# Kernel tuning notes

Measured on AMD Instinct MI355X. Metric: run time of the kernel, lower is better.

Reference implementation:

```python
import jax, jax.numpy as jnp
import numpy as np

NEG_SLOPE = 0.01  # torch F.leaky_relu default


def _leaky_relu(v):
    return jnp.where(v >= 0, v, NEG_SLOPE * v)


def _att_layer(t, w1, w2):
    # t: [b, c, n] ; SE-style channel attention with scalar gate
    y = t.mean(axis=-1)                                   # [b, c] (AdaptiveAvgPool1d(1))
    y = jax.nn.sigmoid(jax.nn.relu(y @ w1.T) @ w2.T)       # [b, 1]
    return t * y[:, :, None]


def _avwgcn(x, node_emb, supports, cheb, wpool, bpool, iw, ib, gw, gb,
            a1w1, a1w2, a2w1, a2w2):
    # x: [b, n, c_in]; supports/cheb: [k, n, n]
    b, n, _ = x.shape
    weights = jnp.einsum('nd,dkio->nkio', node_emb, wpool)   # per-node dyn weights
    bias = node_emb @ bpool                                  # [n, o]
    x_g = jnp.einsum('knm,bmc->bnkc', supports, x)           # [b, n, k, c_in]
    x_gconv0 = jnp.einsum('bnki,nkio->bno', x_g, weights) + bias
    x0 = x @ iw.T + ib                                       # init_gconv: [b, n, o]
    x_g1 = jnp.einsum('knm,bmc->bnkc', cheb, x0).reshape(b, n, -1)
    x_gconv1 = x_g1 @ gw.T + gb                              # [b, n, o]
    out = (_att_layer(_leaky_relu(x_gconv0).transpose(0, 2, 1), a1w1, a1w2)
           + _att_layer(_leaky_relu(x_gconv1).transpose(0, 2, 1), a2w1, a2w2))
    return out.transpose(0, 2, 1)                            # [b, n, o]


def _cheb_supports(L, k):
    n = L.shape[0]
    s = [jnp.eye(n, dtype=L.dtype), L]
    for _ in range(2, k):
        s.append(2.0 * L @ s[-1] - s[-2])
    return jnp.stack(s, axis=0)  # [k, n, n]


B, N, DIN, DOUT, K, ED = 64, 1024, 32, 64, 3, 16
CIN = DIN + DOUT  # 96 (gate/update input = cat(x, state))


def setup_inputs() -> dict:
    key = jax.random.key(0)
    ks = jax.random.split(key, 32)
    g = lambda i, shape, s=0.1: jax.random.normal(ks[i], shape, dtype=jnp.float32) * s
    inp = {
        'x': jax.random.normal(ks[0], (B, N, DIN), dtype=jnp.float32),
        'state': jax.random.normal(ks[1], (B, N, DOUT), dtype=jnp.float32),
        'node_embeddings': jax.random.normal(ks[2], (N, ED), dtype=jnp.float32),
        'learned_tilde': jax.random.normal(ks[3], (N, N), dtype=jnp.float32) / np.sqrt(N),
        'cheb_polynomials': jax.random.normal(ks[4], (K, N, N), dtype=jnp.float32) / np.sqrt(N),
        # gate AVWGCN: dim_in=96, dim_out=2*DOUT=128
        'gate_wpool': g(5, (ED, K, CIN, 2 * DOUT)),
        'gate_bpool': g(6, (ED, 2 * DOUT)),
        'gate_iw': g(7, (2 * DOUT, CIN)), 'gate_ib': g(8, (2 * DOUT,)),
        'gate_gw': g(9, (2 * DOUT, 2 * DOUT * K)), 'gate_gb': g(10, (2 * DOUT,)),
        'gate_a1w1': g(11, (2 * DOUT // 16, 2 * DOUT)), 'gate_a1w2': g(12, (1, 2 * DOUT // 16)),
        'gate_a2w1': g(13, (2 * DOUT // 16, 2 * DOUT)), 'gate_a2w2': g(14, (1, 2 * DOUT // 16)),
        # update AVWGCN: dim_in=96, dim_out=DOUT=64
        'upd_wpool': g(15, (ED, K, CIN, DOUT)),
        'upd_bpool': g(16, (ED, DOUT)),
        'upd_iw': g(17, (DOUT, CIN)), 'upd_ib': g(18, (DOUT,)),
        'upd_gw': g(19, (DOUT, DOUT * K)), 'upd_gb': g(20, (DOUT,)),
        'upd_a1w1': g(21, (DOUT // 16, DOUT)), 'upd_a1w2': g(22, (1, DOUT // 16)),
        'upd_a2w1': g(23, (DOUT // 16, DOUT)), 'upd_a2w2': g(24, (1, DOUT // 16)),
    }
    return inp


def reference(x, state, node_embeddings, learned_tilde, cheb_polynomials,
              gate_wpool, gate_bpool, gate_iw, gate_ib, gate_gw, gate_gb,
              gate_a1w1, gate_a1w2, gate_a2w1, gate_a2w2,
              upd_wpool, upd_bpool, upd_iw, upd_ib, upd_gw, upd_gb,
              upd_a1w1, upd_a1w2, upd_a2w1, upd_a2w2):
    supports = _cheb_supports(learned_tilde, K)  # [k, n, n]
    inp_state = jnp.concatenate([x, state], axis=-1)  # [b, n, din+dout]
    z_r = jax.nn.sigmoid(_avwgcn(inp_state, node_embeddings, supports, cheb_polynomials,
                                 gate_wpool, gate_bpool, gate_iw, gate_ib, gate_gw, gate_gb,
                                 gate_a1w1, gate_a1w2, gate_a2w1, gate_a2w2))
    z, r = jnp.split(z_r, 2, axis=-1)
    candidate = jnp.concatenate([x, z * state], axis=-1)
    hc = jnp.tanh(_avwgcn(candidate, node_embeddings, supports, cheb_polynomials,
                          upd_wpool, upd_bpool, upd_iw, upd_ib, upd_gw, upd_gb,
                          upd_a1w1, upd_a1w2, upd_a2w1, upd_a2w2))
    h = r * state + (1.0 - r) * hc
    return h
```

## Files before the change

kernel.cpp:

```cpp
#include <hip/hip_runtime.h>
#include <hip/hip_bf16.h>
#include <math.h>


#define B_  64
#define N_  1024
#define CIN_ 96
#define R_  288

typedef __attribute__((ext_vector_type(8))) short bf16x8;
typedef __attribute__((ext_vector_type(4))) float f32x4;
typedef unsigned short u16;
typedef unsigned int u32;

__device__ __forceinline__ float lrelu(float v) { return v >= 0.f ? v : 0.01f * v; }
__device__ __forceinline__ float sigmoidf_(float u) { return 1.f / (1.f + expf(-u)); }
__device__ __forceinline__ u16 f2b(float f) {
  union { float f; u32 u; } c; c.f = f;
  u32 u = c.u;
  return (u16)((u + 0x7FFFu + ((u >> 16) & 1u)) >> 16);
}
__device__ __forceinline__ float b2f(u16 u) {
  union { u32 x; float f; } c; c.x = ((u32)u) << 16; return c.f;
}
__device__ __forceinline__ void gload_lds16(const u16* gp, u16* lp) {
  __builtin_amdgcn_global_load_lds((const __attribute__((address_space(1))) u32*)gp,
                                   (__attribute__((address_space(3))) u32*)lp, 16, 0, 0);
}

__global__ __launch_bounds__(256) void concat_bf2(const float* __restrict__ x,
                                                  const float* __restrict__ st,
                                                  float* __restrict__ inp,
                                                  u16* __restrict__ inpb) {
  size_t t = (size_t)blockIdx.x * 256 + threadIdx.x;
  if (t >= (size_t)B_ * N_ * CIN_) return;
  int i = (int)(t % CIN_);
  size_t v = t / CIN_;
  size_t b = v & 63, n = v >> 6;
  float f = (i < 32) ? x[(b * N_ + n) * 32 + i] : st[(b * N_ + n) * 64 + (i - 32)];
  inp[t] = f;
  inpb[t] = f2b(f);
}

__global__ __launch_bounds__(256) void conv_f2b(const float* __restrict__ in,
                                                u16* __restrict__ out, int n4) {
  int t = blockIdx.x * 256 + threadIdx.x;
  if (t >= n4) return;
  float4 v = ((const float4*)in)[t];
  ushort4 o;
  o.x = f2b(v.x); o.y = f2b(v.y); o.z = f2b(v.z); o.w = f2b(v.w);
  ((ushort4*)out)[t] = o;
}

__global__ __launch_bounds__(256) void split_hilo(const float* __restrict__ in,
                                                  u16* __restrict__ hi,
                                                  u16* __restrict__ lo, int n4) {
  int t = blockIdx.x * 256 + threadIdx.x;
  if (t >= n4) return;
  float4 v = ((const float4*)in)[t];
  ushort4 h, l;
  h.x = f2b(v.x); l.x = f2b(v.x - b2f(h.x));
  h.y = f2b(v.y); l.y = f2b(v.y - b2f(h.y));
  h.z = f2b(v.z); l.z = f2b(v.z - b2f(h.z));
  h.w = f2b(v.w); l.w = f2b(v.w - b2f(h.w));
  ((ushort4*)hi)[t] = h;
  ((ushort4*)lo)[t] = l;
}

__global__ __launch_bounds__(256) void transpose_split(const float* __restrict__ in,
                                                       u16* __restrict__ hiT,
                                                       u16* __restrict__ loT) {
  __shared__ float t[32][33];
  const int tid = threadIdx.x;
  const int j0 = blockIdx.x * 32, r0 = blockIdx.y * 32;
  const int tc = tid & 31, tr = tid >> 5;
#pragma unroll
  for (int q = 0; q < 4; ++q)
    t[tr + q * 8][tc] = in[(size_t)(r0 + tr + q * 8) * 1024 + j0 + tc];
  __syncthreads();
  const int jj = tid >> 3, rq = (tid & 7) * 4;
  ushort4 h, l;
#pragma unroll
  for (int q = 0; q < 4; ++q) {
    float v = t[rq + q][jj];
    u16 hh = f2b(v);
    ((u16*)&h)[q] = hh;
    ((u16*)&l)[q] = f2b(v - b2f(hh));
  }
  *(ushort4*)(hiT + (size_t)(j0 + jj) * N_ + r0 + rq) = h;
  *(ushort4*)(loT + (size_t)(j0 + jj) * N_ + r0 + rq) = l;
}

__global__ __launch_bounds__(256) void transpose_b2b(const u16* __restrict__ Z, int Zs,
                                                     int Ctot, u16* __restrict__ Zt) {
  __shared__ u16 t[32][36];
  const int tid = threadIdx.x;
  const int c0 = blockIdx.x * 32, n0 = blockIdx.y * 32, b = blockIdx.z;
  {
    const int i = tid >> 3, c4 = (tid & 7) * 4;
    ushort4 v = *(const ushort4*)(Z + ((size_t)(n0 + i) * 64 + b) * Zs + c0 + c4);
    t[i][c4] = v.x; t[i][c4 + 1] = v.y; t[i][c4 + 2] = v.z; t[i][c4 + 3] = v.w;
  }
  __syncthreads();
  {
    const int c = tid >> 3, n4 = (tid & 7) * 4;
    ushort4 o;
    o.x = t[n4][c]; o.y = t[n4 + 1][c]; o.z = t[n4 + 2][c]; o.w = t[n4 + 3][c];
    *(ushort4*)(Zt + (size_t)(b * Ctot + c0 + c) * 1024 + n0 + n4) = o;
  }
}

__global__ __launch_bounds__(256) void mfma_l2p(const u16* __restrict__ Lhi,
                                                const u16* __restrict__ Llo,
                                                const u16* __restrict__ LhiT,
                                                const u16* __restrict__ LloT,
                                                float* __restrict__ P) {
  __shared__ u16 Asl[64 * 64];
  __shared__ u16 Bsl[64 * 64];
  const int tid = threadIdx.x;
  const int w = tid >> 6, lane = tid & 63;
  const int m0 = blockIdx.y * 64, n0 = blockIdx.x * 64;
  const int ph = blockIdx.z;
  const int wr = w >> 1, wc = w & 1;
  const int sr = lane >> 3, so = lane & 7;
  const int cl = lane & 15, q4 = lane >> 4;
  f32x4 acc[2][2] = {};

  const u16* A = (ph == 1) ? Llo : Lhi;
  const u16* B = (ph == 2) ? LloT : LhiT;
  for (int k0 = 0; k0 < 1024; k0 += 64) {
    __syncthreads();
#pragma unroll
    for (int i = 0; i < 2; ++i) {
      const int r = i * 32 + w * 8 + sr;
      const int o = so ^ (r & 7);
      gload_lds16(A + (size_t)(m0 + r) * 1024 + k0 + o * 8, Asl + (i * 32 + w * 8) * 64);
      gload_lds16(B + (size_t)(n0 + r) * 1024 + k0 + o * 8, Bsl + (i * 32 + w * 8) * 64);
    }
    __syncthreads();
#pragma unroll
    for (int kk = 0; kk < 2; ++kk) {
      bf16x8 af[2], bfr[2];
#pragma unroll
      for (int mi = 0; mi < 2; ++mi) {
        const int ra = wr * 32 + mi * 16 + cl;
        af[mi] = *(const bf16x8*)(Asl + ra * 64 + ((kk * 4 + q4) ^ (ra & 7)) * 8);
      }
#pragma unroll
      for (int ni = 0; ni < 2; ++ni) {
        const int rb = wc * 32 + ni * 16 + cl;
        bfr[ni] = *(const bf16x8*)(Bsl + rb * 64 + ((kk * 4 + q4) ^ (rb & 7)) * 8);
      }
#pragma unroll
      for (int mi = 0; mi < 2; ++mi)
#pragma unroll
        for (int ni = 0; ni < 2; ++ni)
          acc[mi][ni] = __builtin_amdgcn_mfma_f32_16x16x32_bf16(af[mi], bfr[ni], acc[mi][ni], 0, 0, 0);
    }
  }
  float* Pz = P + ((size_t)ph << 20);
#pragma unroll
  for (int mi = 0; mi < 2; ++mi)
#pragma unroll
    for (int ni = 0; ni < 2; ++ni) {
      const int j = n0 + wc * 32 + ni * 16 + cl;
#pragma unroll
      for (int r = 0; r < 4; ++r) {
        const int m = m0 + wr * 32 + mi * 16 + q4 * 4 + r;
        Pz[(size_t)m * 1024 + j] = acc[mi][ni][r];
      }
    }
}

__global__ __launch_bounds__(256) void l2_finish(const float* __restrict__ P,
                                                 u16* __restrict__ Y) {
  int t = blockIdx.x * 256 + threadIdx.x;
  float4 a = ((const float4*)P)[t];
  float4 b = ((const float4*)(P + 1048576))[t];
  float4 c = ((const float4*)(P + 2097152))[t];
  int e = t << 2;
  int m = e >> 10, j = e & 1023;
  ushort4 o;
  o.x = f2b(2.f * (a.x + b.x + c.x) - (m == j     ? 1.f : 0.f));
  o.y = f2b(2.f * (a.y + b.y + c.y) - (m == j + 1 ? 1.f : 0.f));
  o.z = f2b(2.f * (a.z + b.z + c.z) - (m == j + 2 ? 1.f : 0.f));
  o.w = f2b(2.f * (a.w + b.w + c.w) - (m == j + 3 ? 1.f : 0.f));
  ((ushort4*)Y)[t] = o;
}

__global__ __launch_bounds__(256) void mfma_stack_f32(const u16* __restrict__ A,
                                                      const u16* __restrict__ Bt,
                                                      float* __restrict__ Y, int J) {
  __shared__ u16 Asl[2][128 * 32];
  __shared__ u16 Bsl[2][128 * 32];
  const int tid = threadIdx.x;
  const int w = tid >> 6, lane = tid & 63;
  const int m0 = blockIdx.y * 128, n0 = blockIdx.x * 128;
  const int wr = w >> 1, wc = w & 1;
  const int sr = lane >> 2, so = lane & 3;
  const int cl = lane & 15, q4 = lane >> 4;
  f32x4 acc[4][4] = {};

  auto STAGE = [&](u16* Ad, u16* Bd, int k0) {
#pragma unroll
    for (int i = 0; i < 2; ++i) {
      const int r = i * 64 + w * 16 + sr;
      const int o = so ^ ((r >> 1) & 3);
      gload_lds16(A + (size_t)(m0 + r) * 1024 + k0 + o * 8, Ad + (i * 64 + w * 16) * 32);
      gload_lds16(Bt + (size_t)(n0 + r) * 1024 + k0 + o * 8, Bd + (i * 64 + w * 16) * 32);
    }
  };
  auto COMPUTE = [&](const u16* As, const u16* Bs) {
    bf16x8 af[4], bfr[4];
#pragma unroll
    for (int mi = 0; mi < 4; ++mi) {
      const int ra = wr * 64 + mi * 16 + cl;
      af[mi] = *(const bf16x8*)(As + ra * 32 + (q4 ^ ((ra >> 1) & 3)) * 8);
    }
#pragma unroll
    for (int ni = 0; ni < 4; ++ni) {
      const int rb = wc * 64 + ni * 16 + cl;
      bfr[ni] = *(const bf16x8*)(Bs + rb * 32 + (q4 ^ ((rb >> 1) & 3)) * 8);
    }
#pragma unroll
    for (int mi = 0; mi < 4; ++mi)
#pragma unroll
      for (int ni = 0; ni < 4; ++ni)
        acc[mi][ni] = __builtin_amdgcn_mfma_f32_16x16x32_bf16(af[mi], bfr[ni], acc[mi][ni], 0, 0, 0);
  };

  STAGE(Asl[0], Bsl[0], 0);
  for (int k0 = 0; k0 < 1024; k0 += 64) {
    STAGE(Asl[1], Bsl[1], k0 + 32);
    asm volatile("s_waitcnt vmcnt(4)" ::: "memory");
    __builtin_amdgcn_s_barrier();
    __builtin_amdgcn_sched_barrier(0);
    COMPUTE(Asl[0], Bsl[0]);
    asm volatile("s_waitcnt lgkmcnt(0)" ::: "memory");
    __builtin_amdgcn_s_barrier();
    __builtin_amdgcn_sched_barrier(0);
    if (k0 + 64 < 1024) {
      STAGE(Asl[0], Bsl[0], k0 + 64);
      asm volatile("s_waitcnt vmcnt(4)" ::: "memory");
    } else {
      asm volatile("s_waitcnt vmcnt(0)" ::: "memory");
    }
    __builtin_amdgcn_s_barrier();
    __builtin_amdgcn_sched_barrier(0);
    COMPUTE(Asl[1], Bsl[1]);
    asm volatile("s_waitcnt lgkmcnt(0)" ::: "memory");
    __builtin_amdgcn_s_barrier();
    __builtin_amdgcn_sched_barrier(0);
  }
#pragma unroll
  for (int mi = 0; mi < 4; ++mi)
#pragma unroll
    for (int ni = 0; ni < 4; ++ni) {
      const int j = n0 + wc * 64 + ni * 16 + cl;
#pragma unroll
      for (int r = 0; r < 4; ++r) {
        const int m = m0 + wr * 64 + mi * 16 + q4 * 4 + r;
        Y[(size_t)m * J + j] = acc[mi][ni][r];
      }
    }
}

template <int O, int OSH>
__global__ __launch_bounds__(128) void vgen2(const float* __restrict__ gw,
                                             const float* __restrict__ iw,
                                             const float* __restrict__ ib,
                                             int Ctot,
                                             u16* __restrict__ Vb,
                                             float* __restrict__ ball) {
  const int c = blockIdx.x;
  const int col = threadIdx.x;
  if (c >= Ctot) {
    if (col < 96) Vb[(size_t)c * 96 + col] = 0;
    else if (col == 96) ball[c] = 0.f;
    return;
  }
  __shared__ float sg[O];
  const int o = c & (O - 1), k = c >> OSH;
  const float* g = gw + (size_t)o * (3 * O) + (size_t)k * O;
  for (int e = col; e < O; e += 128) sg[e] = g[e];
  __syncthreads();
  if (col < 96) {
    float s = 0.f;
#pragma unroll
    for (int j = 0; j < O; ++j) s += sg[j] * iw[j * 96 + col];
    Vb[(size_t)c * 96 + col] = f2b(s);
  } else if (col == 96) {
    float s = 0.f;
#pragma unroll
    for (int j = 0; j < O; ++j) s += sg[j] * ib[j];
    ball[c] = s;
  }
}

__global__ __launch_bounds__(256) void zgemm(const u16* __restrict__ A,
                                             const u16* __restrict__ Bt,
                                             const float* __restrict__ ball,
                                             u16* __restrict__ Z, int Zs) {
  __shared__ u16 Asl[128 * 32];
  __shared__ u16 Bsl[128 * 32];
  const int tid = threadIdx.x;
  const int w = tid >> 6, lane = tid & 63;
  const int m0 = blockIdx.y * 128, n0 = blockIdx.x * 128;
  const int wr = w >> 1, wc = w & 1;
  const int sr = lane >> 2, so = lane & 3;
  const int cl = lane & 15, q4 = lane >> 4;
  f32x4 acc[4][4] = {};
  for (int k0 = 0; k0 < 96; k0 += 32) {
    __syncthreads();
#pragma unroll
    for (int i = 0; i < 2; ++i) {
      const int r = i * 64 + w * 16 + sr;
      const int o = so ^ (r & 3);
      gload_lds16(A + (size_t)(m0 + r) * 96 + k0 + o * 8, Asl + (i * 64 + w * 16) * 32);
      gload_lds16(Bt + (size_t)(n0 + r) * 96 + k0 + o * 8, Bsl + (i * 64 + w * 16) * 32);
    }
    __syncthreads();
    bf16x8 af[4], bfr[4];
#pragma unroll
    for (int mi = 0; mi < 4; ++mi) {
      const int ra = wr * 64 + mi * 16 + cl;
      af[mi] = *(const bf16x8*)(Asl + ra * 32 + (q4 ^ (ra & 3)) * 8);
    }
#pragma unroll
    for (int ni = 0; ni < 4; ++ni) {
      const int rb = wc * 64 + ni * 16 + cl;
      bfr[ni] = *(const bf16x8*)(Bsl + rb * 32 + (q4 ^ (rb & 3)) * 8);
    }
#pragma unroll
    for (int mi = 0; mi < 4; ++mi)
#pragma unroll
      for (int ni = 0; ni < 4; ++ni)
        acc[mi][ni] = __builtin_amdgcn_mfma_f32_16x16x32_bf16(af[mi], bfr[ni], acc[mi][ni], 0, 0, 0);
  }
#pragma unroll
  for (int mi = 0; mi < 4; ++mi)
#pragma unroll
    for (int ni = 0; ni < 4; ++ni) {
      const int c = n0 + wc * 64 + ni * 16 + cl;
      const float bb = ball[c];
#pragma unroll
      for (int r = 0; r < 4; ++r) {
        const int m = m0 + wr * 64 + mi * 16 + q4 * 4 + r;
        Z[(size_t)m * Zs + c] = f2b(acc[mi][ni][r] + bb);
      }
    }
}

__global__ __launch_bounds__(512) void mfma_k3(const u16* __restrict__ A3,
                                               const u16* __restrict__ Zt,
                                               const float* __restrict__ gb,
                                               float* __restrict__ Y,
                                               int J, int obits) {
  __shared__ u16 Asl[2][128 * 64];
  __shared__ u16 Bsl[2][128 * 64];
  const int tid = threadIdx.x;
  const int w = tid >> 6, lane = tid & 63;
  const int m0 = blockIdx.y * 128, n0 = blockIdx.x * 128;
  const int wr = w >> 2, wc = w & 3;
  const int sr = lane >> 3, so = lane & 7;
  const int cl = lane & 15, q4 = lane >> 4;
  const int omask = (1 << obits) - 1;
  f32x4 acc[4][2] = {};

  auto STAGE = [&](u16* Ad, u16* Bd, int k0) {
    const int kb = k0 >> 10, ko = k0 & 1023;
#pragma unroll
    for (int i = 0; i < 2; ++i) {
      const int r = i * 64 + w * 8 + sr;
      const int o = so ^ (r & 7);
      gload_lds16(A3 + (size_t)kb * 1048576 + (size_t)(m0 + r) * 1024 + ko + o * 8,
                  Ad + (i * 64 + w * 8) * 64);
      const int jp = n0 + r;
      const int brow = (((jp >> obits) * 3 + kb) << obits) | (jp & omask);
      gload_lds16(Zt + (size_t)brow * 1024 + ko + o * 8, Bd + (i * 64 + w * 8) * 64);
    }
  };
  auto COMPUTE = [&](const u16* As, const u16* Bs) {
#pragma unroll
    for (int kk = 0; kk < 2; ++kk) {
      bf16x8 af[4], bfr[2];
#pragma unroll
      for (int mi = 0; mi < 4; ++mi) {
        const int ra = wr * 64 + mi * 16 + cl;
        af[mi] = *(const bf16x8*)(As + ra * 64 + ((kk * 4 + q4) ^ (ra & 7)) * 8);
      }
#pragma unroll
      for (int ni = 0; ni < 2; ++ni) {
        const int rb = wc * 32 + ni * 16 + cl;
        bfr[ni] = *(const bf16x8*)(Bs + rb * 64 + ((kk * 4 + q4) ^ (rb & 7)) * 8);
      }
#pragma unroll
      for (int mi = 0; mi < 4; ++mi)
#pragma unroll
        for (int ni = 0; ni < 2; ++ni)
          acc[mi][ni] = __builtin_amdgcn_mfma_f32_16x16x32_bf16(af[mi], bfr[ni], acc[mi][ni], 0, 0, 0);
    }
  };

  STAGE(Asl[0], Bsl[0], 0);
  for (int k0 = 0; k0 < 3072; k0 += 128) {
    STAGE(Asl[1], Bsl[1], k0 + 64);
    asm volatile("s_waitcnt vmcnt(4)" ::: "memory");
    __builtin_amdgcn_s_barrier();
    __builtin_amdgcn_sched_barrier(0);
    COMPUTE(Asl[0], Bsl[0]);
    asm volatile("s_waitcnt lgkmcnt(0)" ::: "memory");
    __builtin_amdgcn_s_barrier();
    __builtin_amdgcn_sched_barrier(0);
    if (k0 + 128 < 3072) {
      STAGE(Asl[0], Bsl[0], k0 + 128);
      asm volatile("s_waitcnt vmcnt(4)" ::: "memory");
    } else {
      asm volatile("s_waitcnt vmcnt(0)" ::: "memory");
    }
    __builtin_amdgcn_s_barrier();
    __builtin_amdgcn_sched_barrier(0);
    COMPUTE(Asl[1], Bsl[1]);
    asm volatile("s_waitcnt lgkmcnt(0)" ::: "memory");
    __builtin_amdgcn_s_barrier();
    __builtin_amdgcn_sched_barrier(0);
  }
#pragma unroll
  for (int mi = 0; mi < 4; ++mi)
#pragma unroll
    for (int ni = 0; ni < 2; ++ni) {
      const int j = n0 + wc * 32 + ni * 16 + cl;
      const float bb = gb[j & omask];
#pragma unroll
      for (int r = 0; r < 4; ++r) {
        const int m = m0 + wr * 64 + mi * 16 + q4 * 4 + r;
        Y[(size_t)m * J + j] = acc[mi][ni][r] + bb;
      }
    }
}

__global__ __launch_bounds__(512) void mfma_k3w(const u16* __restrict__ A3,
                                                const u16* __restrict__ Zt,
                                                const float* __restrict__ gb,
                                                float* __restrict__ Y,
                                                int J, int obits) {
  __shared__ u16 Asl[2][128 * 64];
  __shared__ u16 Bsl[2][256 * 64];
  const int tid = threadIdx.x;
  const int w = tid >> 6, lane = tid & 63;
  const int m0 = blockIdx.y * 128, n0 = blockIdx.x * 256;
  const int wr = w >> 2, wc = w & 3;
  const int sr = lane >> 3, so = lane & 7;
  const int cl = lane & 15, q4 = lane >> 4;
  const int omask = (1 << obits) - 1;
  f32x4 acc[4][4] = {};

  auto STAGE = [&](u16* Ad, u16* Bd, int k0) {
    const int kb = k0 >> 10, ko = k0 & 1023;
#pragma unroll
    for (int i = 0; i < 2; ++i) {
      const int r = i * 64 + w * 8 + sr;
      const int o = so ^ (r & 7);
      gload_lds16(A3 + (size_t)kb * 1048576 + (size_t)(m0 + r) * 1024 + ko + o * 8,
                  Ad + (i * 64 + w * 8) * 64);
    }
#pragma unroll
    for (int i = 0; i < 4; ++i) {
      const int r = i * 64 + w * 8 + sr;
      const int o = so ^ (r & 7);
      const int jp = n0 + r;
      const int brow = (((jp >> obits) * 3 + kb) << obits) | (jp & omask);
      gload_lds16(Zt + (size_t)brow * 1024 + ko + o * 8, Bd + (i * 64 + w * 8) * 64);
    }
  };
  auto COMPUTE = [&](const u16* As, const u16* Bs) {
#pragma unroll
    for (int kk = 0; kk < 2; ++kk) {
      bf16x8 af[4], bfr[4];
#pragma unroll
      for (int mi = 0; mi < 4; ++mi) {
        const int ra = wr * 64 + mi * 16 + cl;
        af[mi] = *(const bf16x8*)(As + ra * 64 + ((kk * 4 + q4) ^ (ra & 7)) * 8);
      }
#pragma unroll
      for (int ni = 0; ni < 4; ++ni) {
        const int rb = wc * 64 + ni * 16 + cl;
        bfr[ni] = *(const bf16x8*)(Bs + rb * 64 + ((kk * 4 + q4) ^ (rb & 7)) * 8);
      }
#pragma unroll
      for (int mi = 0; mi < 4; ++mi)
#pragma unroll
        for (int ni = 0; ni < 4; ++ni)
          acc[mi][ni] = __builtin_amdgcn_mfma_f32_16x16x32_bf16(af[mi], bfr[ni], acc[mi][ni], 0, 0, 0);
    }
  };

  STAGE(Asl[0], Bsl[0], 0);
  for (int k0 = 0; k0 < 3072; k0 += 128) {
    STAGE(Asl[1], Bsl[1], k0 + 64);
    asm volatile("s_waitcnt vmcnt(6)" ::: "memory");
    __builtin_amdgcn_s_barrier();
    __builtin_amdgcn_sched_barrier(0);
    COMPUTE(Asl[0], Bsl[0]);
    asm volatile("s_waitcnt lgkmcnt(0)" ::: "memory");
    __builtin_amdgcn_s_barrier();
    __builtin_amdgcn_sched_barrier(0);
    if (k0 + 128 < 3072) {
      STAGE(Asl[0], Bsl[0], k0 + 128);
      asm volatile("s_waitcnt vmcnt(6)" ::: "memory");
    } else {
      asm volatile("s_waitcnt vmcnt(0)" ::: "memory");
    }
    __builtin_amdgcn_s_barrier();
    __builtin_amdgcn_sched_barrier(0);
    COMPUTE(Asl[1], Bsl[1]);
    asm volatile("s_waitcnt lgkmcnt(0)" ::: "memory");
    __builtin_amdgcn_s_barrier();
    __builtin_amdgcn_sched_barrier(0);
  }
#pragma unroll
  for (int mi = 0; mi < 4; ++mi)
#pragma unroll
    for (int ni = 0; ni < 4; ++ni) {
      const int j = n0 + wc * 64 + ni * 16 + cl;
      const float bb = gb[j & omask];
#pragma unroll
      for (int r = 0; r < 4; ++r) {
        const int m = m0 + wr * 64 + mi * 16 + q4 * 4 + r;
        Y[(size_t)m * J + j] = acc[mi][ni][r] + bb;
      }
    }
}

template <int OW>
__global__ __launch_bounds__(256) void weightgen3w(const float* __restrict__ emb,
                                                   const float* __restrict__ wpool,
                                                   u16* __restrict__ W) {
  const int tid = threadIdx.x;
  const int ro = blockIdx.x * 256 + tid;
  const int r = ro / OW, o = ro % OW;
  const int n0 = blockIdx.y * 64;
  __shared__ float semb[64][17];
  for (int e = tid; e < 1024; e += 256) semb[e >> 4][e & 15] = emb[(n0 + (e >> 4)) * 16 + (e & 15)];
  __syncthreads();
  float wv[16];
#pragma unroll
  for (int d = 0; d < 16; ++d) wv[d] = wpool[((size_t)d * R_ + r) * OW + o];
#pragma unroll 4
  for (int n = 0; n < 64; ++n) {
    float s = 0.f;
#pragma unroll
    for (int d = 0; d < 16; ++d) s += semb[n][d] * wv[d];
    W[(size_t)(n0 + n) * (R_ * OW) + ro] = f2b(s);
  }
}

template <int OW>
__global__ __launch_bounds__(256) void pernode9(const float* __restrict__ xa,
                                                const float* __restrict__ xbc,
                                                const u16* __restrict__ W,
                                                const float* __restrict__ emb,
                                                const float* __restrict__ bpool,
                                                float* __restrict__ outp) {
  constexpr int QO = OW / 32;
  const int n = blockIdx.x;
  const int tid = threadIdx.x;
  __shared__ __align__(16) float sW[32][OW + 4];
  __shared__ __align__(16) float sX[32][68];
  __shared__ float semb[16];
  if (tid < 16) semb[tid] = emb[n * 16 + tid];
  const int tx = tid & 31, tb = tid >> 5;
  const int lb = tid >> 2, li = (tid & 3) * 8;
  float acc[8][QO] = {};
  const u16* Wn = W + (size_t)n * (R_ * OW);

  for (int c = 0; c < 9; ++c) {
    const int k = c / 3, i0 = (c % 3) * 32;
    const float* xk = (k == 0) ? (xa + (size_t)n * 6144)
                               : (xbc + ((size_t)(k - 1) * 1024 + n) * 6144);
    __syncthreads();
    {
#pragma unroll
      for (int it = 0; it < OW / 64; ++it) {
        const int slot = it * 256 + tid;
        const int row = slot / (OW / 8), o8 = (slot % (OW / 8)) * 8;
        uint4 v = *(const uint4*)(Wn + (size_t)(c * 32 + row) * OW + o8);
        sW[row][o8 + 0] = b2f((u16)(v.x & 0xFFFF)); sW[row][o8 + 1] = b2f((u16)(v.x >> 16));
        sW[row][o8 + 2] = b2f((u16)(v.y & 0xFFFF)); sW[row][o8 + 3] = b2f((u16)(v.y >> 16));
        sW[row][o8 + 4] = b2f((u16)(v.z & 0xFFFF)); sW[row][o8 + 5] = b2f((u16)(v.z >> 16));
        sW[row][o8 + 6] = b2f((u16)(v.w & 0xFFFF)); sW[row][o8 + 7] = b2f((u16)(v.w >> 16));
      }
    }
    {
      const float* p = xk + (size_t)lb * 96 + i0 + li;
      float4 v0 = *(const float4*)p;
      float4 v1 = *(const float4*)(p + 4);
      sX[li + 0][lb] = v0.x; sX[li + 1][lb] = v0.y;
      sX[li + 2][lb] = v0.z; sX[li + 3][lb] = v0.w;
      sX[li + 4][lb] = v1.x; sX[li + 5][lb] = v1.y;
      sX[li + 6][lb] = v1.z; sX[li + 7][lb] = v1.w;
    }
    __syncthreads();
#pragma unroll
    for (int il = 0; il < 32; ++il) {
      float4 xv0 = *(const float4*)&sX[il][tb * 8];
      float4 xv1 = *(const float4*)&sX[il][tb * 8 + 4];
      float xv[8] = {xv0.x, xv0.y, xv0.z, xv0.w, xv1.x, xv1.y, xv1.z, xv1.w};
      float wv[QO];
      if constexpr (QO == 4) {
        float4 w4 = *(const float4*)&sW[il][tx * 4];
        wv[0] = w4.x; wv[1] = w4.y; wv[2] = w4.z; wv[3] = w4.w;
      } else {
        float2 w2 = *(const float2*)&sW[il][tx * 2];
        wv[0] = w2.x; wv[1] = w2.y;
      }
#pragma unroll
      for (int j = 0; j < 8; ++j)
#pragma unroll
        for (int q = 0; q < QO; ++q) acc[j][q] += xv[j] * wv[q];
    }
  }
  float bias[QO];
#pragma unroll
  for (int q = 0; q < QO; ++q) {
    int o = tx * QO + q;
    float s = 0.f;
#pragma unroll
    for (int d = 0; d < 16; ++d) s += semb[d] * bpool[d * OW + o];
    bias[q] = s;
  }
#pragma unroll
  for (int j = 0; j < 8; ++j) {
    size_t base = ((size_t)n * B_ + tb * 8 + j) * OW + tx * QO;
#pragma unroll
    for (int q = 0; q < QO; ++q) outp[base + q] = acc[j][q] + bias[q];
  }
}

template <int C>
__global__ __launch_bounds__(256) void att_reduce(const float* __restrict__ A0,
                                                  const float* __restrict__ A1,
                                                  float* __restrict__ part0,
                                                  float* __restrict__ part1) {
  constexpr int C4 = C / 4;
  constexpr int H = 256 / C4;
  const int chunk = blockIdx.x;
  const int b = blockIdx.y;
  const int tid = threadIdx.x;
  const int c4 = tid % C4, h = tid / C4;
  __shared__ float4 r0[256], r1[256];
  float4 s0 = {0.f, 0.f, 0.f, 0.f}, s1 = {0.f, 0.f, 0.f, 0.f};
  const float4* p0 = (const float4*)(A0 + (size_t)b * C) + c4;
  const float4* p1 = (const float4*)(A1 + (size_t)b * C) + c4;
  const size_t stride = (size_t)B_ * C4;
  for (int n = chunk * 64 + h; n < chunk * 64 + 64; n += H) {
    float4 v0 = p0[(size_t)n * stride];
    float4 v1 = p1[(size_t)n * stride];
    s0.x += lrelu(v0.x); s0.y += lrelu(v0.y); s0.z += lrelu(v0.z); s0.w += lrelu(v0.w);
    s1.x += lrelu(v1.x); s1.y += lrelu(v1.y); s1.z += lrelu(v1.z); s1.w += lrelu(v1.w);
  }
  r0[tid] = s0; r1[tid] = s1;
  __syncthreads();
  if (h == 0) {
    for (int hh = 1; hh < H; ++hh) {
      float4 a = r0[c4 + hh * C4], bb = r1[c4 + hh * C4];
      s0.x += a.x; s0.y += a.y; s0.z += a.z; s0.w += a.w;
      s1.x += bb.x; s1.y += bb.y; s1.z += bb.z; s1.w += bb.w;
    }
    ((float4*)(part0 + ((size_t)b * 16 + chunk) * C))[c4] = s0;
    ((float4*)(part1 + ((size_t)b * 16 + chunk) * C))[c4] = s1;
  }
}

template <int C, int HID>
__global__ __launch_bounds__(256) void att_finish(const float* __restrict__ part0,
                                                  const float* __restrict__ part1,
                                                  const float* __restrict__ w11,
                                                  const float* __restrict__ w12,
                                                  const float* __restrict__ w21,
                                                  const float* __restrict__ w22,
                                                  float* __restrict__ sout) {
  const int b = blockIdx.x;
  const int tid = threadIdx.x;
  __shared__ float sm0[C], sm1[C];
  __shared__ float h0[HID], h1[HID];
  if (tid < C) {
    float s0 = 0.f, s1 = 0.f;
    for (int ch = 0; ch < 16; ++ch) {
      s0 += part0[((size_t)b * 16 + ch) * C + tid];
      s1 += part1[((size_t)b * 16 + ch) * C + tid];
    }
    sm0[tid] = s0 * (1.f / N_); sm1[tid] = s1 * (1.f / N_);
  }
  __syncthreads();
  if (tid < HID) {
    float a = 0.f;
    for (int cc = 0; cc < C; ++cc) a += sm0[cc] * w11[tid * C + cc];
    h0[tid] = fmaxf(a, 0.f);
  } else if (tid >= 32 && tid < 32 + HID) {
    int j = tid - 32;
    float a = 0.f;
    for (int cc = 0; cc < C; ++cc) a += sm1[cc] * w21[j * C + cc];
    h1[j] = fmaxf(a, 0.f);
  }
  __syncthreads();
  if (tid == 0) {
    float a = 0.f;
    for (int j = 0; j < HID; ++j) a += h0[j] * w12[j];
    sout[b] = sigmoidf_(a);
  } else if (tid == 32) {
    float a = 0.f;
    for (int j = 0; j < HID; ++j) a += h1[j] * w22[j];
    sout[B_ + b] = sigmoidf_(a);
  }
}

__global__ __launch_bounds__(256) void gate_combine_b2(const float* __restrict__ a0,
                                                       const float* __restrict__ a1,
                                                       const float* __restrict__ s12,
                                                       const float* __restrict__ x,
                                                       const float* __restrict__ st,
                                                       float* __restrict__ cand,
                                                       u16* __restrict__ candb,
                                                       float* __restrict__ rbuf) {
  size_t t = (size_t)blockIdx.x * 256 + threadIdx.x;
  if (t >= (size_t)B_ * N_ * 64) return;
  int c = (int)(t & 63);
  int b = (int)((t >> 6) & 63);
  int n = (int)(t >> 12);
  float s1 = s12[b], s2 = s12[B_ + b];
  size_t nb = (size_t)n * B_ + b;
  size_t i128 = nb * 128;
  float uz = s1 * lrelu(a0[i128 + c]) + s2 * lrelu(a1[i128 + c]);
  float ur = s1 * lrelu(a0[i128 + 64 + c]) + s2 * lrelu(a1[i128 + 64 + c]);
  float z = sigmoidf_(uz);
  float r = sigmoidf_(ur);
  float stv = st[((size_t)b * N_ + n) * 64 + c];
  float zs = z * stv;
  cand[nb * CIN_ + 32 + c] = zs;
  candb[nb * CIN_ + 32 + c] = f2b(zs);
  rbuf[nb * 64 + c] = r;
  if (c < 32) {
    float xv = x[((size_t)b * N_ + n) * 32 + c];
    cand[nb * CIN_ + c] = xv;
    candb[nb * CIN_ + c] = f2b(xv);
  }
}

__global__ __launch_bounds__(256) void final_h(const float* __restrict__ a0,
                                               const float* __restrict__ a1,
                                               const float* __restrict__ s12,
                                               const float* __restrict__ rbuf,
                                               const float* __restrict__ st,
                                               float* __restrict__ out) {
  size_t t = (size_t)blockIdx.x * 256 + threadIdx.x;
  if (t >= (size_t)B_ * N_ * 64) return;
  int o = (int)(t & 63);
  int n = (int)((t >> 6) & 1023);
  int b = (int)(t >> 16);
  float s1 = s12[b], s2 = s12[B_ + b];
  size_t nb = ((size_t)n * B_ + b) * 64 + o;
  float u = s1 * lrelu(a0[nb]) + s2 * lrelu(a1[nb]);
  float hc = tanhf(u);
  float r = rbuf[nb];
  out[t] = r * st[t] + (1.f - r) * hc;
}

extern "C" void kernel_launch(void* const* d_in, const int* in_sizes, int n_in,
                              void* d_out, int out_size, void* d_ws, size_t ws_size,
                              hipStream_t stream) {
  const float* x       = (const float*)d_in[0];
  const float* state   = (const float*)d_in[1];
  const float* emb     = (const float*)d_in[2];
  const float* Ltil    = (const float*)d_in[3];
  const float* cheb    = (const float*)d_in[4];
  const float* g_wpool = (const float*)d_in[5];
  const float* g_bpool = (const float*)d_in[6];
  const float* g_iw    = (const float*)d_in[7];
  const float* g_ib    = (const float*)d_in[8];
  const float* g_gw    = (const float*)d_in[9];
  const float* g_gb    = (const float*)d_in[10];
  const float* g_a1w1  = (const float*)d_in[11];
  const float* g_a1w2  = (const float*)d_in[12];
  const float* g_a2w1  = (const float*)d_in[13];
  const float* g_a2w2  = (const float*)d_in[14];
  const float* u_wpool = (const float*)d_in[15];
  const float* u_bpool = (const float*)d_in[16];
  const float* u_iw    = (const float*)d_in[17];
  const float* u_ib    = (const float*)d_in[18];
  const float* u_gw    = (const float*)d_in[19];
  const float* u_gb    = (const float*)d_in[20];
  const float* u_a1w1  = (const float*)d_in[21];
  const float* u_a1w2  = (const float*)d_in[22];
  const float* u_a2w1  = (const float*)d_in[23];
  const float* u_a2w2  = (const float*)d_in[24];
  float* out = (float*)d_out;

  float* ws    = (float*)d_ws;
  float* inp   = ws;
  u16*   inpb  = (u16*)(ws + 6291456);
  float* t12   = ws + 9437184;
  u16*   Zbuf  = (u16*)t12;
  u16*   Wbuf  = (u16*)(ws + 22020096);
  u16*   Wbuf128 = Wbuf;
  u16*   Btp   = (u16*)(ws + 31457280);
  u16*   Zt    = Wbuf;
  float* acc1  = ws + 34603008;
  float* acc0  = ws + 42991616;
  u16*   LbStk = (u16*)(ws + 51380224);
  u16*   chebb = (u16*)(ws + 52428800);
  float* s12   = ws + 54001664;
  float* s12u  = ws + 54001792;
  float* part0 = ws + 54001920;
  float* part1 = ws + 54132992;
  float* rbuf  = ws + 54264064;
  u16*   Vbg   = (u16*)(ws + 58458368);
  float* bag   = ws + 58476800;
  u16*   Vbu   = (u16*)(ws + 58477184);
  float* bau   = ws + 58489472;
  u16*   LhiT  = (u16*)(ws + 58489728);
  u16*   LloT  = (u16*)(ws + 59014016);
  u16*   Llo   = (u16*)(ws + 59538304);

  dim3 blk(256);
  dim3 blk512(512);

  split_hilo<<<1024, blk, 0, stream>>>(Ltil, LbStk, Llo, 262144);
  transpose_split<<<dim3(32, 32), blk, 0, stream>>>(Ltil, LhiT, LloT);
  mfma_l2p<<<dim3(16, 16, 3), blk, 0, stream>>>(LbStk, Llo, LhiT, LloT, t12);
  l2_finish<<<1024, blk, 0, stream>>>(t12, LbStk + 1048576);
  conv_f2b<<<3072, blk, 0, stream>>>(cheb, chebb, 786432);

  concat_bf2<<<24576, blk, 0, stream>>>(x, state, inp, inpb);
  transpose_b2b<<<dim3(3, 32, 64), blk, 0, stream>>>(inpb, 96, 96, Btp);
  mfma_stack_f32<<<dim3(48, 16), blk, 0, stream>>>(LbStk, Btp, t12, 6144);
  vgen2<128, 7><<<384, dim3(128), 0, stream>>>(g_gw, g_iw, g_ib, 384, Vbg, bag);
  weightgen3w<128><<<dim3(144, 16), blk, 0, stream>>>(emb, g_wpool, Wbuf128);
  pernode9<128><<<1024, blk, 0, stream>>>(inp, t12, Wbuf128, emb, g_bpool, acc0);
  zgemm<<<dim3(3, 512), blk, 0, stream>>>(inpb, Vbg, bag, Zbuf, 384);
  transpose_b2b<<<dim3(12, 32, 64), blk, 0, stream>>>(Zbuf, 384, 384, Zt);
  mfma_k3w<<<dim3(32, 8), blk512, 0, stream>>>(chebb, Zt, g_gb, acc1, 8192, 7);
  att_reduce<128><<<dim3(16, 64), blk, 0, stream>>>(acc0, acc1, part0, part1);
  att_finish<128, 8><<<64, blk, 0, stream>>>(part0, part1, g_a1w1, g_a1w2, g_a2w1, g_a2w2, s12);
  gate_combine_b2<<<16384, blk, 0, stream>>>(acc0, acc1, s12, x, state, inp, inpb, rbuf);

  transpose_b2b<<<dim3(3, 32, 64), blk, 0, stream>>>(inpb, 96, 96, Btp);
  mfma_stack_f32<<<dim3(48, 16), blk, 0, stream>>>(LbStk, Btp, t12, 6144);
  vgen2<64, 6><<<256, dim3(128), 0, stream>>>(u_gw, u_iw, u_ib, 192, Vbu, bau);
  weightgen3w<64><<<dim3(72, 16), blk, 0, stream>>>(emb, u_wpool, Wbuf);
  pernode9<64><<<1024, blk, 0, stream>>>(inp, t12, Wbuf, emb, u_bpool, acc0);
  zgemm<<<dim3(2, 512), blk, 0, stream>>>(inpb, Vbu, bau, Zbuf, 256);
  transpose_b2b<<<dim3(6, 32, 64), blk, 0, stream>>>(Zbuf, 256, 192, Zt);
  mfma_k3<<<dim3(32, 8), blk512, 0, stream>>>(chebb, Zt, u_gb, acc1, 4096, 6);
  att_reduce<64><<<dim3(16, 64), blk, 0, stream>>>(acc0, acc1, part0, part1);
  att_finish<64, 4><<<64, blk, 0, stream>>>(part0, part1, u_a1w1, u_a1w2, u_a2w1, u_a2w2, s12u);
  final_h<<<16384, blk, 0, stream>>>(acc0, acc1, s12u, rbuf, state, out);
}
```

Before: 714.9 us.

## Widen stacked support GEMM to 128x256 tiles with 512 threads and K=64 stages

The bf16 MFMA GEMM that applies the stacked supports to the node features now uses 8 waves per block, a 128x256 output tile and a 64-wide K stage. The LDS swizzle changes from 4 to 8 chunks per row. The aim is more reuse of each staged A tile, fewer barriers per K, and half as many blocks. Separately, the per-node weight staging writes LDS as two float4 stores instead of eight scalar stores. The cost is more LDS per block (96KB double-buffered) and only 384 blocks, which could lower occupancy and leave some CUs idle.

```diff
diff --git a/kernel.cpp b/kernel.cpp
--- a/kernel.cpp
+++ b/kernel.cpp
@@ -188,60 +188,68 @@
   ((ushort4*)Y)[t] = o;
 }
 
-__global__ __launch_bounds__(256) void mfma_stack_f32(const u16* __restrict__ A,
-                                                      const u16* __restrict__ Bt,
-                                                      float* __restrict__ Y, int J) {
-  __shared__ u16 Asl[2][128 * 32];
-  __shared__ u16 Bsl[2][128 * 32];
+__global__ __launch_bounds__(512) void mfma_stack_w(const u16* __restrict__ A,
+                                                    const u16* __restrict__ Bt,
+                                                    float* __restrict__ Y, int J) {
+  __shared__ u16 Asl[2][128 * 64];
+  __shared__ u16 Bsl[2][256 * 64];
   const int tid = threadIdx.x;
   const int w = tid >> 6, lane = tid & 63;
-  const int m0 = blockIdx.y * 128, n0 = blockIdx.x * 128;
-  const int wr = w >> 1, wc = w & 1;
-  const int sr = lane >> 2, so = lane & 3;
+  const int m0 = blockIdx.y * 128, n0 = blockIdx.x * 256;
+  const int wr = w >> 2, wc = w & 3;
+  const int sr = lane >> 3, so = lane & 7;
   const int cl = lane & 15, q4 = lane >> 4;
   f32x4 acc[4][4] = {};
 
   auto STAGE = [&](u16* Ad, u16* Bd, int k0) {
 #pragma unroll
     for (int i = 0; i < 2; ++i) {
-      const int r = i * 64 + w * 16 + sr;
-      const int o = so ^ ((r >> 1) & 3);
-      gload_lds16(A + (size_t)(m0 + r) * 1024 + k0 + o * 8, Ad + (i * 64 + w * 16) * 32);
-      gload_lds16(Bt + (size_t)(n0 + r) * 1024 + k0 + o * 8, Bd + (i * 64 + w * 16) * 32);
+      const int r = i * 64 + w * 8 + sr;
+      const int o = so ^ (r & 7);
+      gload_lds16(A + (size_t)(m0 + r) * 1024 + k0 + o * 8, Ad + (i * 64 + w * 8) * 64);
+    }
+#pragma unroll
+    for (int i = 0; i < 4; ++i) {
+      const int r = i * 64 + w * 8 + sr;
+      const int o = so ^ (r & 7);
+      gload_lds16(Bt + (size_t)(n0 + r) * 1024 + k0 + o * 8, Bd + (i * 64 + w * 8) * 64);
     }
   };
   auto COMPUTE = [&](const u16* As, const u16* Bs) {
-    bf16x8 af[4], bfr[4];
-#pragma unroll
-    for (int mi = 0; mi < 4; ++mi) {
-      const int ra = wr * 64 + mi * 16 + cl;
-      af[mi] = *(const bf16x8*)(As + ra * 32 + (q4 ^ ((ra >> 1) & 3)) * 8);
-    }
-#pragma unroll
-    for (int ni = 0; ni < 4; ++ni) {
-      const int rb = wc * 64 + ni * 16 + cl;
-      bfr[ni] = *(const bf16x8*)(Bs + rb * 32 + (q4 ^ ((rb >> 1) & 3)) * 8);
-    }
-#pragma unroll
-    for (int mi = 0; mi < 4; ++mi)
-#pragma unroll
-      for (int ni = 0; ni < 4; ++ni)
-        acc[mi][ni] = __builtin_amdgcn_mfma_f32_16x16x32_bf16(af[mi], bfr[ni], acc[mi][ni], 0, 0, 0);
+#pragma unroll
+    for (int kk = 0; kk < 2; ++kk) {
+      bf16x8 af[4], bfr[4];
+#pragma unroll
+      for (int mi = 0; mi < 4; ++mi) {
+        const int ra = wr * 64 + mi * 16 + cl;
+        af[mi] = *(const bf16x8*)(As + ra * 64 + ((kk * 4 + q4) ^ (ra & 7)) * 8);
+      }
+#pragma unroll
+      for (int ni = 0; ni < 4; ++ni) {
+        const int rb = wc * 64 + ni * 16 + cl;
+        bfr[ni] = *(const bf16x8*)(Bs + rb * 64 + ((kk * 4 + q4) ^ (rb & 7)) * 8);
+      }
+#pragma unroll
+      for (int mi = 0; mi < 4; ++mi)
+#pragma unroll
+        for (int ni = 0; ni < 4; ++ni)
+          acc[mi][ni] = __builtin_amdgcn_mfma_f32_16x16x32_bf16(af[mi], bfr[ni], acc[mi][ni], 0, 0, 0);
+    }
   };
 
   STAGE(Asl[0], Bsl[0], 0);
-  for (int k0 = 0; k0 < 1024; k0 += 64) {
-    STAGE(Asl[1], Bsl[1], k0 + 32);
-    asm volatile("s_waitcnt vmcnt(4)" ::: "memory");
+  for (int k0 = 0; k0 < 1024; k0 += 128) {
+    STAGE(Asl[1], Bsl[1], k0 + 64);
+    asm volatile("s_waitcnt vmcnt(6)" ::: "memory");
     __builtin_amdgcn_s_barrier();
     __builtin_amdgcn_sched_barrier(0);
     COMPUTE(Asl[0], Bsl[0]);
     asm volatile("s_waitcnt lgkmcnt(0)" ::: "memory");
     __builtin_amdgcn_s_barrier();
     __builtin_amdgcn_sched_barrier(0);
-    if (k0 + 64 < 1024) {
-      STAGE(Asl[0], Bsl[0], k0 + 64);
-      asm volatile("s_waitcnt vmcnt(4)" ::: "memory");
+    if (k0 + 128 < 1024) {
+      STAGE(Asl[0], Bsl[0], k0 + 128);
+      asm volatile("s_waitcnt vmcnt(6)" ::: "memory");
     } else {
       asm volatile("s_waitcnt vmcnt(0)" ::: "memory");
     }
@@ -585,10 +593,13 @@
         const int slot = it * 256 + tid;
         const int row = slot / (OW / 8), o8 = (slot % (OW / 8)) * 8;
         uint4 v = *(const uint4*)(Wn + (size_t)(c * 32 + row) * OW + o8);
-        sW[row][o8 + 0] = b2f((u16)(v.x & 0xFFFF)); sW[row][o8 + 1] = b2f((u16)(v.x >> 16));
-        sW[row][o8 + 2] = b2f((u16)(v.y & 0xFFFF)); sW[row][o8 + 3] = b2f((u16)(v.y >> 16));
-        sW[row][o8 + 4] = b2f((u16)(v.z & 0xFFFF)); sW[row][o8 + 5] = b2f((u16)(v.z >> 16));
-        sW[row][o8 + 6] = b2f((u16)(v.w & 0xFFFF)); sW[row][o8 + 7] = b2f((u16)(v.w >> 16));
+        float4 f0, f1;
+        f0.x = b2f((u16)(v.x & 0xFFFF)); f0.y = b2f((u16)(v.x >> 16));
+        f0.z = b2f((u16)(v.y & 0xFFFF)); f0.w = b2f((u16)(v.y >> 16));
+        f1.x = b2f((u16)(v.z & 0xFFFF)); f1.y = b2f((u16)(v.z >> 16));
+        f1.z = b2f((u16)(v.w & 0xFFFF)); f1.w = b2f((u16)(v.w >> 16));
+        *(float4*)&sW[row][o8] = f0;
+        *(float4*)&sW[row][o8 + 4] = f1;
       }
     }
     {
@@ -833,7 +844,7 @@
 
   concat_bf2<<<24576, blk, 0, stream>>>(x, state, inp, inpb);
   transpose_b2b<<<dim3(3, 32, 64), blk, 0, stream>>>(inpb, 96, 96, Btp);
-  mfma_stack_f32<<<dim3(48, 16), blk, 0, stream>>>(LbStk, Btp, t12, 6144);
+  mfma_stack_w<<<dim3(24, 16), blk512, 0, stream>>>(LbStk, Btp, t12, 6144);
   vgen2<128, 7><<<384, dim3(128), 0, stream>>>(g_gw, g_iw, g_ib, 384, Vbg, bag);
   weightgen3w<128><<<dim3(144, 16), blk, 0, stream>>>(emb, g_wpool, Wbuf128);
   pernode9<128><<<1024, blk, 0, stream>>>(inp, t12, Wbuf128, emb, g_bpool, acc0);
@@ -845,7 +856,7 @@
   gate_combine_b2<<<16384, blk, 0, stream>>>(acc0, acc1, s12, x, state, inp, inpb, rbuf);
 
   transpose_b2b<<<dim3(3, 32, 64), blk, 0, stream>>>(inpb, 96, 96, Btp);
-  mfma_stack_f32<<<dim3(48, 16), blk, 0, stream>>>(LbStk, Btp, t12, 6144);
+  mfma_stack_w<<<dim3(24, 16), blk512, 0, stream>>>(LbStk, Btp, t12, 6144);
   vgen2<64, 6><<<256, dim3(128), 0, stream>>>(u_gw, u_iw, u_ib, 192, Vbu, bau);
   weightgen3w<64><<<dim3(72, 16), blk, 0, stream>>>(emb, u_wpool, Wbuf);
   pernode9<64><<<1024, blk, 0, stream>>>(inp, t12, Wbuf, emb, u_bpool, acc0);
```

Result: faster. 695.8 us (-2.7%).
